# Kernel tuning notes

Measured on AMD Instinct MI355X. Metric: run time of the kernel, lower is better.

Reference implementation:

```python
import jax, jax.numpy as jnp
import numpy as np

B, S, M, D, DI, H, DH, DFF = 2, 1024, 1024, 1024, 1024, 16, 64, 4096
NEG = -1e30


def _ln(x, g, b, eps=1e-5):
    mu = jnp.mean(x, -1, keepdims=True)
    var = jnp.mean((x - mu) ** 2, -1, keepdims=True)
    return (x - mu) / jnp.sqrt(var + eps) * g + b


def _rel_shift(x):
    # x: (b, i, j, h) -- Transformer-XL shift via pad + reshape (exact torch trick)
    b, i, j, h = x.shape
    zp = jnp.zeros((b, 1, j, h), x.dtype)
    xp = jnp.concatenate([zp, x], axis=1).reshape(i + 1, b, j, h)
    return xp[1:].reshape(b, i, j, h)


def setup_inputs() -> dict:
    key = jax.random.key(0)
    ks = jax.random.split(key, 24)
    rn = lambda k, sh, s=1.0: jax.random.normal(k, sh, jnp.float32) * s
    St = S + M
    causal = jnp.arange(St)[None, :] > (jnp.arange(S)[:, None] + M)  # (S, St)
    tgt_mask = jnp.broadcast_to(causal[None, :, :, None], (B, S, St, 1))
    return {
        "x": rn(ks[0], (B, S, D)),
        "enc_output": rn(ks[1], (B, S, D)),
        "pos_emb": rn(ks[2], (St, DI)),
        "u": rn(ks[3], (H, DH), 0.02),
        "v": rn(ks[4], (H, DH), 0.02),
        "mem": rn(ks[5], (B, M, D)),
        "tgt_mask": tgt_mask,
        "Wq_m": rn(ks[6], (D, DI), 0.02),
        "Wkv_m": rn(ks[7], (D, 2 * DI), 0.02),
        "fcw_m": rn(ks[8], (DI, D), 0.02),
        "fcb_m": jnp.zeros((D,), jnp.float32),
        "lnm_g": jnp.ones((D,), jnp.float32),
        "lnm_b": jnp.zeros((D,), jnp.float32),
        "Wq_c": rn(ks[9], (D, DI), 0.02),
        "Wkv_c": rn(ks[10], (D, 2 * DI), 0.02),
        "fcw_c": rn(ks[11], (DI, D), 0.02),
        "fcb_c": jnp.zeros((D,), jnp.float32),
        "lnc_g": jnp.ones((D,), jnp.float32),
        "lnc_b": jnp.zeros((D,), jnp.float32),
        "W1": rn(ks[12], (D, DFF), 0.02),
        "b1": jnp.zeros((DFF,), jnp.float32),
        "W2": rn(ks[13], (DFF, D), 0.02),
        "b2": jnp.zeros((D,), jnp.float32),
        "ln1_g": jnp.ones((D,), jnp.float32),
        "ln1_b": jnp.zeros((D,), jnp.float32),
        "ln2_g": jnp.ones((D,), jnp.float32),
        "ln2_b": jnp.zeros((D,), jnp.float32),
        "ln3_g": jnp.ones((D,), jnp.float32),
        "ln3_b": jnp.zeros((D,), jnp.float32),
    }


def reference(x, enc_output, pos_emb, u, v, mem, tgt_mask,
              Wq_m, Wkv_m, fcw_m, fcb_m, lnm_g, lnm_b,
              Wq_c, Wkv_c, fcw_c, fcb_c, lnc_g, lnc_b,
              W1, b1, W2, b2,
              ln1_g, ln1_b, ln2_g, ln2_b, ln3_g, ln3_b):
    scale = 1.0 / (DH ** 0.5)

    def mha(xn):  # RecurrenceAttention (internal post-norm, pre_norm=False)
        h = jnp.concatenate([mem, xn], axis=1)                       # (B, M+S, D)
        q = (xn @ Wq_m).reshape(B, S, H, DH)
        k, vv = jnp.split(h @ Wkv_m, 2, axis=-1)
        k = k.reshape(B, S + M, H, DH)
        vv = vv.reshape(B, S + M, H, DH)
        content = jnp.einsum('bihd,bjhd->bijh', q + u, k)
        pe = pos_emb.reshape(S + M, H, DH)
        pos = jnp.einsum('bihd,jhd->bijh', q + v, pe)
        attn = content + _rel_shift(pos)
        attn = jnp.where(tgt_mask, NEG, attn)
        attn = attn * scale
        attn = jax.nn.softmax(attn, axis=1)                          # NOTE: query axis (faithful)
        o = jnp.einsum('bijh,bjhd->bihd', attn, vv).reshape(B, S, DI)
        return _ln(xn + o @ fcw_m + fcb_m, lnm_g, lnm_b)

    def cross(dec):  # CrossAttention (internal post-norm)
        q = (dec @ Wq_c).reshape(B, S, H, DH)
        k, vv = jnp.split(enc_output @ Wkv_c, 2, axis=-1)
        k = k.reshape(B, S, H, DH)
        vv = vv.reshape(B, S, H, DH)
        attn = jnp.einsum('bihd,bjhd->bijh', q, k) * scale
        attn = jax.nn.softmax(attn, axis=1)                          # query axis (faithful)
        o = jnp.einsum('bijh,bjhd->bihd', attn, vv).reshape(B, S, DI)
        return _ln(dec + o @ fcw_c + fcb_c, lnc_g, lnc_b)

    # decoder layer, pre_norm=True path
    out = x + mha(_ln(x, ln1_g, ln1_b))
    out2 = out + cross(_ln(out, ln2_g, ln2_b))
    h = jax.nn.gelu(_ln(out2, ln3_g, ln3_b) @ W1 + b1, approximate=False)
    out3 = out2 + (h @ W2 + b2)
    return out3
```

## Files before the change

### kernel.cpp

```cpp
#include <hip/hip_runtime.h>

typedef unsigned short u16;
typedef __attribute__((ext_vector_type(4))) unsigned short u16x4;
typedef __attribute__((ext_vector_type(8))) unsigned short u16x8;
typedef __attribute__((ext_vector_type(8))) __bf16 bf16x8;
typedef __attribute__((ext_vector_type(4))) float f32x4;

#define DEV __device__ __forceinline__

DEV float b2f(u16 u){ union{ unsigned int i; float f; } x; x.i = ((unsigned int)u) << 16; return x.f; }
DEV u16 f2b(float f){ unsigned int x = __float_as_uint(f); return (u16)((x + 0x7fffu + ((x >> 16) & 1u)) >> 16); }

DEV void block_red2(float& s, float& q){
#pragma unroll
  for (int off = 32; off; off >>= 1){ s += __shfl_down(s, off); q += __shfl_down(q, off); }
  __shared__ float sh1[4], sh2[4];
  int lane = threadIdx.x & 63, w = threadIdx.x >> 6;
  if (lane == 0){ sh1[w] = s; sh2[w] = q; }
  __syncthreads();
  s = sh1[0] + sh1[1] + sh1[2] + sh1[3];
  q = sh2[0] + sh2[1] + sh2[2] + sh2[3];
}

template<int WM, int WN, bool OUTB>
__global__ __launch_bounds__(WM*WN*64) void gemm_bt(
    const u16* __restrict__ A, const u16* __restrict__ Bm, void* __restrict__ Cp,
    int K, int lda, int ldb, int ldc, int Hh,
    long aob, long aoh, long bob, long boh, long cob, long coh)
{
  constexpr int BM = WM*64, BN = WN*64, BK = 64, NW = WM*WN;
  __shared__ u16 At[BM*64];
  __shared__ u16 Bt[BN*64];
  int z = blockIdx.z, b_ = z / Hh, h_ = z % Hh;
  const u16* Ab = A + (long)b_*aob + (long)h_*aoh;
  const u16* Bb = Bm + (long)b_*bob + (long)h_*boh;
  long cbase = (long)b_*cob + (long)h_*coh;
  int m0 = blockIdx.y * BM, n0 = blockIdx.x * BN;
  int tid = threadIdx.x, lane = tid & 63, wv = tid >> 6;
  int wm = wv / WN, wn = wv % WN;
  f32x4 acc[4][4];
  f32x4 z4 = {0.f, 0.f, 0.f, 0.f};
#pragma unroll
  for (int a = 0; a < 4; a++)
#pragma unroll
    for (int b = 0; b < 4; b++) acc[a][b] = z4;
  int lr = lane & 15, lk8 = (lane >> 4) * 8;
  int rq = lane >> 3, cq = (lane & 7) << 3;
  for (int k0 = 0; k0 < K; k0 += BK){
    __syncthreads();
#pragma unroll
    for (int q = wv; q < BM/8; q += NW){
      const u16* g = &Ab[(long)(m0 + q*8 + rq)*lda + k0 + cq];
      __builtin_amdgcn_global_load_lds((const __attribute__((address_space(1))) void*)g,
          (__attribute__((address_space(3))) void*)&At[q*512], 16, 0, 0);
    }
#pragma unroll
    for (int q = wv; q < BN/8; q += NW){
      const u16* g = &Bb[(long)(n0 + q*8 + rq)*ldb + k0 + cq];
      __builtin_amdgcn_global_load_lds((const __attribute__((address_space(1))) void*)g,
          (__attribute__((address_space(3))) void*)&Bt[q*512], 16, 0, 0);
    }
    __syncthreads();
#pragma unroll
    for (int kk = 0; kk < BK; kk += 32){
      bf16x8 af[4], bfr[4];
#pragma unroll
      for (int mi = 0; mi < 4; mi++) af[mi]  = *(bf16x8*)&At[(wm*64 + mi*16 + lr)*64 + kk + lk8];
#pragma unroll
      for (int ni = 0; ni < 4; ni++) bfr[ni] = *(bf16x8*)&Bt[(wn*64 + ni*16 + lr)*64 + kk + lk8];
#pragma unroll
      for (int mi = 0; mi < 4; mi++)
#pragma unroll
        for (int ni = 0; ni < 4; ni++)
          acc[mi][ni] = __builtin_amdgcn_mfma_f32_16x16x32_bf16(af[mi], bfr[ni], acc[mi][ni], 0, 0, 0);
    }
  }
  int orow = (lane >> 4) * 4, ocol = lane & 15;
#pragma unroll
  for (int mi = 0; mi < 4; mi++)
#pragma unroll
    for (int ni = 0; ni < 4; ni++){
      int row = m0 + wm*64 + mi*16 + orow;
      int col = n0 + wn*64 + ni*16 + ocol;
      long cidx = cbase + (long)row*ldc + col;
#pragma unroll
      for (int r = 0; r < 4; r++){
        float vv = acc[mi][ni][r];
        if (OUTB) ((u16*)Cp)[cidx + (long)r*ldc] = f2b(vv);
        else      ((float*)Cp)[cidx + (long)r*ldc] = vv;
      }
    }
}

template<int KD, bool MASK>
__global__ __launch_bounds__(256) void attn_passA(
    const u16* __restrict__ Kp, const u16* __restrict__ Qp, float* __restrict__ mz,
    int J, int kld, int qld,
    long kob, long koh, long qob, long qoh, int H, float scale, int mztot)
{
  constexpr int KP = KD + 8;
  constexpr int RCH = KD / 8;
  constexpr int QREG = KD / 16;
  __shared__ u16 Qt[128*KP];
  int bh = blockIdx.y, b = bh / H, h = bh % H;
  const u16* Kb = Kp + (long)b*kob + (long)h*koh;
  const u16* Qb = Qp + (long)b*qob + (long)h*qoh;
  int j0 = blockIdx.x * 64;
  int tid = threadIdx.x, lane = tid & 63, w = tid >> 6;
  int lr = lane & 15, lk8 = (lane >> 4) * 8;
  bf16x8 ak[KD/32];
  {
    const u16* kr = &Kb[(long)(j0 + w*16 + lr)*kld];
#pragma unroll
    for (int kk = 0; kk < KD/32; kk++) ak[kk] = *(const bf16x8*)&kr[kk*32 + lk8];
  }
  float m_run[4], z_run[4];
#pragma unroll
  for (int r = 0; r < 4; r++){ m_run[r] = -3.0e38f; z_run[r] = 0.f; }
  f32x4 zz = {0.f,0.f,0.f,0.f};
  int itLo = 0;
  if (MASK){ int tt = j0 - 1151; itLo = tt > 0 ? (tt + 127)/128 : 0; }
  u16x8 qreg[QREG];
#pragma unroll
  for (int qq = 0; qq < QREG; qq++){
    int idx = tid + qq*256; int r = idx / RCH, c = (idx % RCH) * 8;
    qreg[qq] = *(const u16x8*)&Qb[(long)(itLo*128 + r)*qld + c];
  }
  for (int it = itLo; it < 8; it++){
    __syncthreads();
#pragma unroll
    for (int qq = 0; qq < QREG; qq++){
      int idx = tid + qq*256; int r = idx / RCH, c = (idx % RCH) * 8;
      *(u16x8*)&Qt[r*KP + c] = qreg[qq];
    }
    if (it + 1 < 8){
#pragma unroll
      for (int qq = 0; qq < QREG; qq++){
        int idx = tid + qq*256; int r = idx / RCH, c = (idx % RCH) * 8;
        qreg[qq] = *(const u16x8*)&Qb[(long)((it+1)*128 + r)*qld + c];
      }
    }
    __syncthreads();
    f32x4 acc[8];
#pragma unroll
    for (int ni = 0; ni < 8; ni++) acc[ni] = zz;
#pragma unroll
    for (int kk = 0; kk < KD; kk += 32){
      bf16x8 bq[8];
#pragma unroll
      for (int ni = 0; ni < 8; ni++) bq[ni] = *(bf16x8*)&Qt[(ni*16 + lr)*KP + kk + lk8];
#pragma unroll
      for (int ni = 0; ni < 8; ni++)
        acc[ni] = __builtin_amdgcn_mfma_f32_16x16x32_bf16(ak[kk/32], bq[ni], acc[ni], 0, 0, 0);
    }
#pragma unroll
    for (int r = 0; r < 4; r++){
      int jg = j0 + w*16 + ((lane >> 4) << 2) + r;
      float sv[8]; float tm = -3.0e38f;
#pragma unroll
      for (int ni = 0; ni < 8; ni++){
        int ig = it*128 + ni*16 + (lane & 15);
        float s = acc[ni][r] * scale;
        bool val = (!MASK) || (ig >= jg - 1024);
        sv[ni] = val ? s : -3.0e38f;
        tm = fmaxf(tm, sv[ni]);
      }
#pragma unroll
      for (int off = 1; off < 16; off <<= 1) tm = fmaxf(tm, __shfl_xor(tm, off));
      float mn = fmaxf(m_run[r], tm);
      float zt = 0.f;
#pragma unroll
      for (int ni = 0; ni < 8; ni++)
        zt += (sv[ni] > -1.0e37f) ? __expf(sv[ni] - mn) : 0.f;
#pragma unroll
      for (int off = 1; off < 16; off <<= 1) zt += __shfl_xor(zt, off);
      z_run[r] = z_run[r] * __expf(m_run[r] - mn) + zt;
      m_run[r] = mn;
    }
  }
  if ((lane & 15) == 0){
#pragma unroll
    for (int r = 0; r < 4; r++){
      int jg = j0 + w*16 + ((lane >> 4) << 2) + r;
      mz[(long)bh*J + jg] = m_run[r];
      mz[(long)mztot + (long)bh*J + jg] = 1.f / z_run[r];
    }
  }
}

template<int KD, bool MASK>
__global__ __launch_bounds__(256) void attn_passB(
    const u16* __restrict__ Kp, const u16* __restrict__ Qp, const u16* __restrict__ Vtp,
    const float* __restrict__ mz, float* __restrict__ Op,
    int J, int kld, int qld, int vld, int oldd,
    long kob, long koh, long qob, long qoh, long vob, long voh, long oob, long ooh,
    int H, float scale, int mztot, int jtHalf, long opstride)
{
  constexpr int KP = KD + 8, PSTR = 140, VSTR = 136;
  constexpr int RCH = KD / 8;
  constexpr int KREG = KD / 16;
  __shared__ u16 PK[128*KP];
  __shared__ u16 Vtt[64*VSTR];
  u16* Kt = PK;
  u16* Pt = PK;
  int bh = blockIdx.y, b = bh / H, h = bh % H;
  int jh = blockIdx.z;
  const u16* Kb = Kp + (long)b*kob + (long)h*koh;
  const u16* Qb = Qp + (long)b*qob + (long)h*qoh;
  const u16* Vb = Vtp + (long)b*vob + (long)h*voh;
  float* Ob = Op + (long)jh*opstride + (long)b*oob + (long)h*ooh;
  const float* mzm = mz + (long)bh*J;
  const float* mzz = mz + (long)mztot + (long)bh*J;
  int i0 = blockIdx.x * 64;
  int tid = threadIdx.x, lane = tid & 63, w = tid >> 6;
  int lr = lane & 15, lk8 = (lane >> 4) * 8;
  bf16x8 aq[KD/32];
  {
    const u16* qr = &Qb[(long)(i0 + w*16 + lr)*qld];
#pragma unroll
    for (int kk = 0; kk < KD/32; kk++) aq[kk] = *(const bf16x8*)&qr[kk*32 + lk8];
  }
  f32x4 acc_o[4];
  f32x4 zz = {0.f,0.f,0.f,0.f};
#pragma unroll
  for (int nd = 0; nd < 4; nd++) acc_o[nd] = zz;
  int lo = jh * jtHalf, hi = lo + jtHalf;
  if (MASK){ int lim = (i0 + 1087)/128 + 1; hi = hi < lim ? hi : lim; }
  if (lo < hi){
    u16x8 kreg[KREG];
    u16x8 vreg[4];
#pragma unroll
    for (int qq = 0; qq < KREG; qq++){
      int idx = tid + qq*256; int r = idx / RCH, c = (idx % RCH) * 8;
      kreg[qq] = *(const u16x8*)&Kb[(long)(lo*128 + r)*kld + c];
    }
#pragma unroll
    for (int qq = 0; qq < 4; qq++){
      int idx = tid + qq*256; int r = idx >> 4, c = (idx & 15) << 3;
      vreg[qq] = *(const u16x8*)&Vb[(long)r*vld + lo*128 + c];
    }
    for (int jt = lo; jt < hi; jt++){
      __syncthreads();
#pragma unroll
      for (int qq = 0; qq < KREG; qq++){
        int idx = tid + qq*256; int r = idx / RCH, c = (idx % RCH) * 8;
        *(u16x8*)&Kt[r*KP + c] = kreg[qq];
      }
#pragma unroll
      for (int qq = 0; qq < 4; qq++){
        int idx = tid + qq*256; int r = idx >> 4, c = (idx & 15) << 3;
        *(u16x8*)&Vtt[r*VSTR + c] = vreg[qq];
      }
      if (jt + 1 < hi){
#pragma unroll
        for (int qq = 0; qq < KREG; qq++){
          int idx = tid + qq*256; int r = idx / RCH, c = (idx % RCH) * 8;
          kreg[qq] = *(const u16x8*)&Kb[(long)((jt+1)*128 + r)*kld + c];
        }
#pragma unroll
        for (int qq = 0; qq < 4; qq++){
          int idx = tid + qq*256; int r = idx >> 4, c = (idx & 15) << 3;
          vreg[qq] = *(const u16x8*)&Vb[(long)r*vld + (jt+1)*128 + c];
        }
      }
      __syncthreads();
      float mjv[8], zjv[8];
#pragma unroll
      for (int ni = 0; ni < 8; ni++){
        int jg = jt*128 + ni*16 + (lane & 15);
        mjv[ni] = mzm[jg]; zjv[ni] = mzz[jg];
      }
      f32x4 acc[8];
#pragma unroll
      for (int ni = 0; ni < 8; ni++) acc[ni] = zz;
#pragma unroll
      for (int kk = 0; kk < KD; kk += 32){
        bf16x8 bk[8];
#pragma unroll
        for (int ni = 0; ni < 8; ni++) bk[ni] = *(bf16x8*)&Kt[(ni*16 + lr)*KP + kk + lk8];
#pragma unroll
        for (int ni = 0; ni < 8; ni++)
          acc[ni] = __builtin_amdgcn_mfma_f32_16x16x32_bf16(aq[kk/32], bk[ni], acc[ni], 0, 0, 0);
      }
      __syncthreads();
#pragma unroll
      for (int ni = 0; ni < 8; ni++){
        int jg = jt*128 + ni*16 + (lane & 15);
#pragma unroll
        for (int r = 0; r < 4; r++){
          int ig = i0 + w*16 + ((lane >> 4) << 2) + r;
          bool val = (!MASK) || (ig >= jg - 1024);
          float p = val ? __expf(acc[ni][r] * scale - mjv[ni]) * zjv[ni] : 0.f;
          Pt[(w*16 + ((lane >> 4) << 2) + r)*PSTR + ni*16 + (lane & 15)] = f2b(p);
        }
      }
#pragma unroll
      for (int kk = 0; kk < 128; kk += 32){
        bf16x8 pa, vb[4];
        pa = *(bf16x8*)&Pt[(w*16 + lr)*PSTR + kk + lk8];
#pragma unroll
        for (int nd = 0; nd < 4; nd++) vb[nd] = *(bf16x8*)&Vtt[(nd*16 + lr)*VSTR + kk + lk8];
#pragma unroll
        for (int nd = 0; nd < 4; nd++)
          acc_o[nd] = __builtin_amdgcn_mfma_f32_16x16x32_bf16(pa, vb[nd], acc_o[nd], 0, 0, 0);
      }
    }
  }
#pragma unroll
  for (int nd = 0; nd < 4; nd++)
#pragma unroll
    for (int r = 0; r < 4; r++){
      int ig = i0 + w*16 + ((lane >> 4) << 2) + r;
      int d = nd*16 + (lane & 15);
      Ob[(long)ig*oldd + d] = acc_o[nd][r];
    }
}

__global__ __launch_bounds__(256) void combine_o(const float* __restrict__ p, u16* __restrict__ o)
{
  const long PS = 2097152;
  long i = ((long)blockIdx.x*256 + threadIdx.x) * 4;
  const float* a = &p[i];
  const float* b = &p[i + PS];
  u16x4 r;
#pragma unroll
  for (int e = 0; e < 4; e++) r[e] = f2b(a[e] + b[e]);
  *(u16x4*)&o[i] = r;
}

__global__ __launch_bounds__(256) void transpose_k(
    const u16* __restrict__ src, u16* __restrict__ dst,
    int lds_, int ldd, int Hh, long sob, long soh, long dob, long doh)
{
  __shared__ u16 tile[64*72];
  int z = blockIdx.z, b_ = z / Hh, h_ = z % Hh;
  const u16* S_ = src + (long)b_*sob + (long)h_*soh;
  u16* D_ = dst + (long)b_*dob + (long)h_*doh;
  int r0 = blockIdx.y * 64, c0 = blockIdx.x * 64;
  int tid = threadIdx.x;
  for (int idx = tid; idx < 512; idx += 256){
    int r = idx >> 3, c = (idx & 7) << 3;
    *(u16x8*)&tile[r*72 + c] = *(const u16x8*)&S_[(long)(r0 + r)*lds_ + c0 + c];
  }
  __syncthreads();
  for (int idx = tid; idx < 512; idx += 256){
    int c = idx >> 3, r = (idx & 7) << 3;
    u16x8 v;
#pragma unroll
    for (int e = 0; e < 8; e++) v[e] = tile[(r + e)*72 + c];
    *(u16x8*)&D_[(long)(c0 + c)*ldd + r0 + r] = v;
  }
}

__global__ __launch_bounds__(256) void transpose_cvt_k(
    const float* __restrict__ src, u16* __restrict__ dst, int lds_, int ldd)
{
  __shared__ u16 tile[64*72];
  int r0 = blockIdx.y * 64, c0 = blockIdx.x * 64;
  int tid = threadIdx.x;
  for (int idx = tid; idx < 512; idx += 256){
    int r = idx >> 3, c = (idx & 7) << 3;
    const float* s = &src[(long)(r0 + r)*lds_ + c0 + c];
#pragma unroll
    for (int e = 0; e < 8; e++) tile[r*72 + c + e] = f2b(s[e]);
  }
  __syncthreads();
  for (int idx = tid; idx < 512; idx += 256){
    int c = idx >> 3, r = (idx & 7) << 3;
    u16x8 v;
#pragma unroll
    for (int e = 0; e < 8; e++) v[e] = tile[(r + e)*72 + c];
    *(u16x8*)&dst[(long)(c0 + c)*ldd + r0 + r] = v;
  }
}

__global__ __launch_bounds__(256) void cvt_k(const float* __restrict__ src, u16* __restrict__ dst)
{
  long i = ((long)blockIdx.x*256 + threadIdx.x) * 4;
  float4 v = *(const float4*)&src[i];
  u16x4 o; o[0] = f2b(v.x); o[1] = f2b(v.y); o[2] = f2b(v.z); o[3] = f2b(v.w);
  *(u16x4*)&dst[i] = o;
}

__global__ __launch_bounds__(256) void ln_k(const float* __restrict__ src, const float* __restrict__ g,
                                            const float* __restrict__ be, u16* __restrict__ out)
{
  long base = (long)blockIdx.x * 1024;
  int tid = threadIdx.x;
  const float* s = src + base + tid*4;
  float v[4] = {s[0], s[1], s[2], s[3]};
  float s1 = v[0]+v[1]+v[2]+v[3];
  float s2 = v[0]*v[0]+v[1]*v[1]+v[2]*v[2]+v[3]*v[3];
  block_red2(s1, s2);
  float mu = s1 * (1.f/1024.f);
  float var = s2 * (1.f/1024.f) - mu*mu;
  float rs = rsqrtf(var + 1e-5f);
#pragma unroll
  for (int e = 0; e < 4; e++){
    int col = tid*4 + e;
    out[base + col] = f2b((v[e]-mu)*rs*g[col] + be[col]);
  }
}

__global__ __launch_bounds__(256) void add_ln_k(const float* __restrict__ go,
    const u16* __restrict__ xn, const float* __restrict__ bias,
    const float* __restrict__ g, const float* __restrict__ be,
    const float* __restrict__ resid, float* __restrict__ outp)
{
  const long PS = 2097152;
// ... 46 lines not shown
  int bj = blockIdx.x;
  int j = bj & 2047;
  long kvrow = (long)bj * 2048;
  long obase = (long)bj * 2048;
  for (int t = threadIdx.x; t < 2048; t += 256){
    int h = t >> 7, e = t & 127;
    u16 val = (e < 64) ? kv[kvrow + h*64 + e] : f2b(pe[(long)j*1024 + h*64 + (e - 64)]);
    BB[obase + t] = val;
  }
}

__global__ __launch_bounds__(256) void gelu_k(const float* __restrict__ f1, const float* __restrict__ b1,
                                              u16* __restrict__ h1)
{
  long i = (long)blockIdx.x*256 + threadIdx.x;
  float x = f1[i] + b1[i & 4095];
  h1[i] = f2b(0.5f * x * (1.f + erff(x * 0.70710678118654752f)));
}

__global__ __launch_bounds__(256) void final_k(const float* __restrict__ out2, const float* __restrict__ f2,
                                               const float* __restrict__ b2v, float* __restrict__ outp)
{
  const long PS = 2097152;
  long i = (long)blockIdx.x*256 + threadIdx.x;
  outp[i] = out2[i] + f2[i] + f2[i + PS] + f2[i + 2*PS] + f2[i + 3*PS] + b2v[i & 1023];
}

extern "C" void kernel_launch(void* const* d_in, const int* in_sizes, int n_in,
                              void* d_out, int out_size, void* d_ws, size_t ws_size,
                              hipStream_t stream)
{
  (void)in_sizes; (void)n_in; (void)out_size; (void)ws_size;
  const float* X    = (const float*)d_in[0];
  const float* ENC  = (const float*)d_in[1];
  const float* PE   = (const float*)d_in[2];
  const float* Uu   = (const float*)d_in[3];
  const float* Vv   = (const float*)d_in[4];
  const float* MEM  = (const float*)d_in[5];
  const float* WQM  = (const float*)d_in[7];
  const float* WKVM = (const float*)d_in[8];
  const float* FCWM = (const float*)d_in[9];
  const float* FCBM = (const float*)d_in[10];
  const float* LNMG = (const float*)d_in[11];
  const float* LNMB = (const float*)d_in[12];
  const float* WQC  = (const float*)d_in[13];
  const float* WKVC = (const float*)d_in[14];
  const float* FCWC = (const float*)d_in[15];
  const float* FCBC = (const float*)d_in[16];
  const float* LNCG = (const float*)d_in[17];
  const float* LNCB = (const float*)d_in[18];
  const float* W1   = (const float*)d_in[19];
  const float* B1   = (const float*)d_in[20];
  const float* W2   = (const float*)d_in[21];
  const float* B2   = (const float*)d_in[22];
  const float* LN1G = (const float*)d_in[23];
  const float* LN1B = (const float*)d_in[24];
  const float* LN2G = (const float*)d_in[25];
  const float* LN2B = (const float*)d_in[26];
  const float* LN3G = (const float*)d_in[27];
  const float* LN3B = (const float*)d_in[28];
  float* OUT = (float*)d_out;
  char* W = (char*)d_ws;
  const size_t MB = 1ull << 20;

  u16*   wT_a  = (u16*)(W + 0*MB);
  u16*   wT_b  = (u16*)(W + 2*MB);
  u16*   wT_c  = (u16*)(W + 6*MB);
  u16*   w1T   = (u16*)(W + 0*MB);
  u16*   xn1   = (u16*)(W + 8*MB);
  u16*   q     = (u16*)(W + 12*MB);
  u16*   o_b   = (u16*)(W + 12*MB);
  u16*   kv    = (u16*)(W + 16*MB);
  float* outb  = (float*)(W + 24*MB);
  u16*   QQ    = (u16*)(W + 32*MB);
  u16*   xn2   = (u16*)(W + 32*MB);
  u16*   qc    = (u16*)(W + 36*MB);
  u16*   BB    = (u16*)(W + 40*MB);
  u16*   kvc   = (u16*)(W + 40*MB);
  u16*   Vtc   = (u16*)(W + 48*MB);
  u16*   oc    = (u16*)(W + 52*MB);
  u16*   Vt    = (u16*)(W + 56*MB);
  u16*   w2T   = (u16*)(W + 56*MB);
  float* mzb   = (float*)(W + 64*MB);
  u16*   memb  = (u16*)(W + 68*MB);
  u16*   encb  = (u16*)(W + 68*MB);
  float* opart = (float*)(W + 66*MB);
  float* ofc   = (float*)(W + 66*MB);
  float* f1    = (float*)(W + 66*MB);
  float* f2    = (float*)(W + 66*MB);
  u16*   h1    = (u16*)(W + 98*MB);
  float* out2b = (float*)(W + 114*MB);

  transpose_cvt_k<<<dim3(16,16),256,0,stream>>>(WQM,  wT_a, 1024,1024);
  transpose_cvt_k<<<dim3(32,16),256,0,stream>>>(WKVM, wT_b, 2048,1024);
  transpose_cvt_k<<<dim3(16,16),256,0,stream>>>(FCWM, wT_c, 1024,1024);
  cvt_k<<<2048,256,0,stream>>>(MEM, memb);
  ln_k<<<2048,256,0,stream>>>(X, LN1G, LN1B, xn1);
  gemm_bt<2,2,true><<<dim3(8,16,1),256,0,stream>>>(xn1, wT_a, q, 1024, 1024,1024,1024, 1, 0,0,0,0,0,0);
  gemm_bt<2,2,true><<<dim3(16,8,2),256,0,stream>>>(memb, wT_b, kv, 1024, 1024,1024,2048, 1,
      1048576,0, 0,0, 4194304,0);
  gemm_bt<2,2,true><<<dim3(16,8,2),256,0,stream>>>(xn1, wT_b, kv + (size_t)1024*2048, 1024, 1024,1024,2048, 1,
      1048576,0, 0,0, 4194304,0);
  build_qq<<<2048,256,0,stream>>>(q, Uu, Vv, QQ);
  build_bb<<<4096,256,0,stream>>>(kv, PE, BB);
  transpose_k<<<dim3(1,32,32),256,0,stream>>>(kv + 1024, Vt, 2048, 2048, 16,
      4194304,64, 2097152,131072);
  attn_passA<128,true><<<dim3(32,32),256,0,stream>>>(BB, QQ, mzb, 2048, 2048, 2048,
      4194304,128, 2097152,128, 16, 0.125f, 65536);
  attn_passB<128,true><<<dim3(16,32,2),256,0,stream>>>(BB, QQ, Vt, mzb, opart, 2048,
      2048,2048,2048,1024, 4194304,128, 2097152,128, 2097152,131072, 1048576,64, 16, 0.125f, 65536,
      8, 2097152);
  combine_o<<<2048,256,0,stream>>>(opart, o_b);
  gemm_bt<2,2,false><<<dim3(8,16,4),256,0,stream>>>(o_b, wT_c, ofc, 256, 1024,1024,1024, 4,
      0,256, 0,256, 0,2097152);
  add_ln_k<<<2048,256,0,stream>>>(ofc, xn1, FCBM, LNMG, LNMB, X, outb);

  transpose_cvt_k<<<dim3(16,16),256,0,stream>>>(WQC,  wT_a, 1024,1024);
  transpose_cvt_k<<<dim3(32,16),256,0,stream>>>(WKVC, wT_b, 2048,1024);
  transpose_cvt_k<<<dim3(16,16),256,0,stream>>>(FCWC, wT_c, 1024,1024);
  cvt_k<<<2048,256,0,stream>>>(ENC, encb);
  ln_k<<<2048,256,0,stream>>>(outb, LN2G, LN2B, xn2);
  gemm_bt<2,2,true><<<dim3(8,16,1),256,0,stream>>>(xn2, wT_a, qc, 1024, 1024,1024,1024, 1, 0,0,0,0,0,0);
  gemm_bt<2,2,true><<<dim3(16,16,1),256,0,stream>>>(encb, wT_b, kvc, 1024, 1024,1024,2048, 1, 0,0,0,0,0,0);
  transpose_k<<<dim3(1,16,32),256,0,stream>>>(kvc + 1024, Vtc, 2048, 1024, 16,
      2097152,64, 1048576,65536);
  attn_passA<64,false><<<dim3(16,32),256,0,stream>>>(kvc, qc, mzb, 1024, 2048, 1024,
      2097152,64, 1048576,64, 16, 0.125f, 32768);
  attn_passB<64,false><<<dim3(16,32,2),256,0,stream>>>(kvc, qc, Vtc, mzb, opart, 1024,
      2048,1024,1024,1024, 2097152,64, 1048576,64, 1048576,65536, 1048576,64, 16, 0.125f, 32768,
      4, 2097152);
  combine_o<<<2048,256,0,stream>>>(opart, oc);
  gemm_bt<2,2,false><<<dim3(8,16,4),256,0,stream>>>(oc, wT_c, ofc, 256, 1024,1024,1024, 4,
      0,256, 0,256, 0,2097152);
  add_ln_k<<<2048,256,0,stream>>>(ofc, xn2, FCBC, LNCG, LNCB, outb, out2b);

  transpose_cvt_k<<<dim3(64,16),256,0,stream>>>(W1, w1T, 4096,1024);
  transpose_cvt_k<<<dim3(16,64),256,0,stream>>>(W2, w2T, 1024,4096);
  ln_k<<<2048,256,0,stream>>>(out2b, LN3G, LN3B, xn2);
  gemm_bt<2,2,false><<<dim3(32,16,1),256,0,stream>>>(xn2, w1T, f1, 1024, 1024,1024,4096, 1, 0,0,0,0,0,0);
  gelu_k<<<32768,256,0,stream>>>(f1, B1, h1);
  gemm_bt<2,2,false><<<dim3(8,16,4),256,0,stream>>>(h1, w2T, f2, 1024, 4096,4096,1024, 4,
      0,1024, 0,1024, 0,2097152);
  final_k<<<8192,256,0,stream>>>(out2b, f2, B2, OUT);
}
```

Before: 676.3 us.

## Double per-wave row tile in attention passes to reuse shared-memory K/Q tiles

Both attention passes now have each wave own 32 rows (two 16-row MFMA subtiles) instead of 16, so each block covers 128 rows and the grids are halved. Every B-operand fragment loaded from LDS (Q, K, V tiles) feeds twice as many MFMAs, cutting LDS and global reloads per unit of work. In exchange, register pressure roughly doubles for accumulators and A fragments, and fewer blocks are launched, which can reduce occupancy and load balance, especially for the causal-masked pass. The P buffer stride was also changed from 140 to 136 so that 128 P rows fit in the shared buffer.

```diff
diff --git a/kernel.cpp b/kernel.cpp
--- a/kernel.cpp
+++ b/kernel.cpp
@@ -105,18 +105,21 @@
   int bh = blockIdx.y, b = bh / H, h = bh % H;
   const u16* Kb = Kp + (long)b*kob + (long)h*koh;
   const u16* Qb = Qp + (long)b*qob + (long)h*qoh;
-  int j0 = blockIdx.x * 64;
+  int j0 = blockIdx.x * 128;
   int tid = threadIdx.x, lane = tid & 63, w = tid >> 6;
   int lr = lane & 15, lk8 = (lane >> 4) * 8;
-  bf16x8 ak[KD/32];
-  {
-    const u16* kr = &Kb[(long)(j0 + w*16 + lr)*kld];
-#pragma unroll
-    for (int kk = 0; kk < KD/32; kk++) ak[kk] = *(const bf16x8*)&kr[kk*32 + lk8];
-  }
-  float m_run[4], z_run[4];
-#pragma unroll
-  for (int r = 0; r < 4; r++){ m_run[r] = -3.0e38f; z_run[r] = 0.f; }
+  bf16x8 ak[2][KD/32];
+#pragma unroll
+  for (int mj = 0; mj < 2; mj++){
+    const u16* kr = &Kb[(long)(j0 + w*32 + mj*16 + lr)*kld];
+#pragma unroll
+    for (int kk = 0; kk < KD/32; kk++) ak[mj][kk] = *(const bf16x8*)&kr[kk*32 + lk8];
+  }
+  float m_run[2][4], z_run[2][4];
+#pragma unroll
+  for (int mj = 0; mj < 2; mj++)
+#pragma unroll
+    for (int r = 0; r < 4; r++){ m_run[mj][r] = -3.0e38f; z_run[mj][r] = 0.f; }
   f32x4 zz = {0.f,0.f,0.f,0.f};
   int itLo = 0;
   if (MASK){ int tt = j0 - 1151; itLo = tt > 0 ? (tt + 127)/128 : 0; }
@@ -141,49 +144,57 @@
       }
     }
     __syncthreads();
-    f32x4 acc[8];
-#pragma unroll
-    for (int ni = 0; ni < 8; ni++) acc[ni] = zz;
-#pragma unroll
-    for (int kk = 0; kk < KD; kk += 32){
+    f32x4 acc[2][8];
+#pragma unroll
+    for (int mj = 0; mj < 2; mj++)
+#pragma unroll
+      for (int ni = 0; ni < 8; ni++) acc[mj][ni] = zz;
+#pragma unroll
+    for (int kk8 = 0; kk8 < KD/32; kk8++){
       bf16x8 bq[8];
 #pragma unroll
-      for (int ni = 0; ni < 8; ni++) bq[ni] = *(bf16x8*)&Qt[(ni*16 + lr)*KP + kk + lk8];
-#pragma unroll
-      for (int ni = 0; ni < 8; ni++)
-        acc[ni] = __builtin_amdgcn_mfma_f32_16x16x32_bf16(ak[kk/32], bq[ni], acc[ni], 0, 0, 0);
-    }
+      for (int ni = 0; ni < 8; ni++) bq[ni] = *(bf16x8*)&Qt[(ni*16 + lr)*KP + kk8*32 + lk8];
+#pragma unroll
+      for (int mj = 0; mj < 2; mj++)
+#pragma unroll
+        for (int ni = 0; ni < 8; ni++)
+          acc[mj][ni] = __builtin_amdgcn_mfma_f32_16x16x32_bf16(ak[mj][kk8], bq[ni], acc[mj][ni], 0, 0, 0);
+    }
+#pragma unroll
+    for (int mj = 0; mj < 2; mj++)
 #pragma unroll
     for (int r = 0; r < 4; r++){
-      int jg = j0 + w*16 + ((lane >> 4) << 2) + r;
+      int jg = j0 + w*32 + mj*16 + ((lane >> 4) << 2) + r;
       float sv[8]; float tm = -3.0e38f;
 #pragma unroll
       for (int ni = 0; ni < 8; ni++){
         int ig = it*128 + ni*16 + (lane & 15);
-        float s = acc[ni][r] * scale;
+        float s = acc[mj][ni][r] * scale;
         bool val = (!MASK) || (ig >= jg - 1024);
         sv[ni] = val ? s : -3.0e38f;
         tm = fmaxf(tm, sv[ni]);
       }
 #pragma unroll
       for (int off = 1; off < 16; off <<= 1) tm = fmaxf(tm, __shfl_xor(tm, off));
-      float mn = fmaxf(m_run[r], tm);
+      float mn = fmaxf(m_run[mj][r], tm);
       float zt = 0.f;
 #pragma unroll
       for (int ni = 0; ni < 8; ni++)
         zt += (sv[ni] > -1.0e37f) ? __expf(sv[ni] - mn) : 0.f;
 #pragma unroll
       for (int off = 1; off < 16; off <<= 1) zt += __shfl_xor(zt, off);
-      z_run[r] = z_run[r] * __expf(m_run[r] - mn) + zt;
-      m_run[r] = mn;
+      z_run[mj][r] = z_run[mj][r] * __expf(m_run[mj][r] - mn) + zt;
+      m_run[mj][r] = mn;
     }
   }
   if ((lane & 15) == 0){
 #pragma unroll
+    for (int mj = 0; mj < 2; mj++)
+#pragma unroll
     for (int r = 0; r < 4; r++){
-      int jg = j0 + w*16 + ((lane >> 4) << 2) + r;
-      mz[(long)bh*J + jg] = m_run[r];
-      mz[(long)mztot + (long)bh*J + jg] = 1.f / z_run[r];
+      int jg = j0 + w*32 + mj*16 + ((lane >> 4) << 2) + r;
+      mz[(long)bh*J + jg] = m_run[mj][r];
+      mz[(long)mztot + (long)bh*J + jg] = 1.f / z_run[mj][r];
     }
   }
 }
@@ -196,10 +207,10 @@
     long kob, long koh, long qob, long qoh, long vob, long voh, long oob, long ooh,
     int H, float scale, int mztot, int jtHalf, long opstride)
 {
-  constexpr int KP = KD + 8, PSTR = 140, VSTR = 136;
+  constexpr int KP = KD + 8, PSTR = 136, VSTR = 136;
   constexpr int RCH = KD / 8;
   constexpr int KREG = KD / 16;
-  __shared__ u16 PK[128*KP];
+  __shared__ u16 PK[128*136];
   __shared__ u16 Vtt[64*VSTR];
   u16* Kt = PK;
   u16* Pt = PK;
@@ -211,19 +222,22 @@
   float* Ob = Op + (long)jh*opstride + (long)b*oob + (long)h*ooh;
   const float* mzm = mz + (long)bh*J;
   const float* mzz = mz + (long)mztot + (long)bh*J;
-  int i0 = blockIdx.x * 64;
+  int i0 = blockIdx.x * 128;
   int tid = threadIdx.x, lane = tid & 63, w = tid >> 6;
   int lr = lane & 15, lk8 = (lane >> 4) * 8;
-  bf16x8 aq[KD/32];
-  {
-    const u16* qr = &Qb[(long)(i0 + w*16 + lr)*qld];
-#pragma unroll
-    for (int kk = 0; kk < KD/32; kk++) aq[kk] = *(const bf16x8*)&qr[kk*32 + lk8];
-  }
-  f32x4 acc_o[4];
+  bf16x8 aq[2][KD/32];
+#pragma unroll
+  for (int mi = 0; mi < 2; mi++){
+    const u16* qr = &Qb[(long)(i0 + w*32 + mi*16 + lr)*qld];
+#pragma unroll
+    for (int kk = 0; kk < KD/32; kk++) aq[mi][kk] = *(const bf16x8*)&qr[kk*32 + lk8];
+  }
+  f32x4 acc_o[2][4];
   f32x4 zz = {0.f,0.f,0.f,0.f};
 #pragma unroll
-  for (int nd = 0; nd < 4; nd++) acc_o[nd] = zz;
+  for (int mi = 0; mi < 2; mi++)
+#pragma unroll
+    for (int nd = 0; nd < 4; nd++) acc_o[mi][nd] = zz;
   int lo = jh * jtHalf, hi = lo + jtHalf;
   if (MASK){ int lim = (i0 + 1087)/128 + 1; hi = hi < lim ? hi : lim; }
   if (lo < hi){
@@ -270,49 +284,60 @@
         int jg = jt*128 + ni*16 + (lane & 15);
         mjv[ni] = mzm[jg]; zjv[ni] = mzz[jg];
       }
-      f32x4 acc[8];
-#pragma unroll
-      for (int ni = 0; ni < 8; ni++) acc[ni] = zz;
-#pragma unroll
-      for (int kk = 0; kk < KD; kk += 32){
+      f32x4 acc[2][8];
+#pragma unroll
+      for (int mi = 0; mi < 2; mi++)
+#pragma unroll
+        for (int ni = 0; ni < 8; ni++) acc[mi][ni] = zz;
+#pragma unroll
+      for (int kk8 = 0; kk8 < KD/32; kk8++){
         bf16x8 bk[8];
 #pragma unroll
-        for (int ni = 0; ni < 8; ni++) bk[ni] = *(bf16x8*)&Kt[(ni*16 + lr)*KP + kk + lk8];
-#pragma unroll
-        for (int ni = 0; ni < 8; ni++)
-          acc[ni] = __builtin_amdgcn_mfma_f32_16x16x32_bf16(aq[kk/32], bk[ni], acc[ni], 0, 0, 0);
+        for (int ni = 0; ni < 8; ni++) bk[ni] = *(bf16x8*)&Kt[(ni*16 + lr)*KP + kk8*32 + lk8];
+#pragma unroll
+        for (int mi = 0; mi < 2; mi++)
+#pragma unroll
+          for (int ni = 0; ni < 8; ni++)
+            acc[mi][ni] = __builtin_amdgcn_mfma_f32_16x16x32_bf16(aq[mi][kk8], bk[ni], acc[mi][ni], 0, 0, 0);
       }
       __syncthreads();
+#pragma unroll
+      for (int mi = 0; mi < 2; mi++)
 #pragma unroll
       for (int ni = 0; ni < 8; ni++){
         int jg = jt*128 + ni*16 + (lane & 15);
 #pragma unroll
         for (int r = 0; r < 4; r++){
-          int ig = i0 + w*16 + ((lane >> 4) << 2) + r;
+          int ig = i0 + w*32 + mi*16 + ((lane >> 4) << 2) + r;
           bool val = (!MASK) || (ig >= jg - 1024);
-          float p = val ? __expf(acc[ni][r] * scale - mjv[ni]) * zjv[ni] : 0.f;
-          Pt[(w*16 + ((lane >> 4) << 2) + r)*PSTR + ni*16 + (lane & 15)] = f2b(p);
+          float p = val ? __expf(acc[mi][ni][r] * scale - mjv[ni]) * zjv[ni] : 0.f;
+          Pt[(w*32 + mi*16 + ((lane >> 4) << 2) + r)*PSTR + ni*16 + (lane & 15)] = f2b(p);
         }
       }
 #pragma unroll
       for (int kk = 0; kk < 128; kk += 32){
-        bf16x8 pa, vb[4];
-        pa = *(bf16x8*)&Pt[(w*16 + lr)*PSTR + kk + lk8];
+        bf16x8 pa[2], vb[4];
 #pragma unroll
         for (int nd = 0; nd < 4; nd++) vb[nd] = *(bf16x8*)&Vtt[(nd*16 + lr)*VSTR + kk + lk8];
 #pragma unroll
-        for (int nd = 0; nd < 4; nd++)
-          acc_o[nd] = __builtin_amdgcn_mfma_f32_16x16x32_bf16(pa, vb[nd], acc_o[nd], 0, 0, 0);
-      }
-    }
-  }
+        for (int mi = 0; mi < 2; mi++) pa[mi] = *(bf16x8*)&Pt[(w*32 + mi*16 + lr)*PSTR + kk + lk8];
+#pragma unroll
+        for (int mi = 0; mi < 2; mi++)
+#pragma unroll
+          for (int nd = 0; nd < 4; nd++)
+            acc_o[mi][nd] = __builtin_amdgcn_mfma_f32_16x16x32_bf16(pa[mi], vb[nd], acc_o[mi][nd], 0, 0, 0);
+      }
+    }
+  }
+#pragma unroll
+  for (int mi = 0; mi < 2; mi++)
 #pragma unroll
   for (int nd = 0; nd < 4; nd++)
 #pragma unroll
     for (int r = 0; r < 4; r++){
-      int ig = i0 + w*16 + ((lane >> 4) << 2) + r;
+      int ig = i0 + w*32 + mi*16 + ((lane >> 4) << 2) + r;
       int d = nd*16 + (lane & 15);
-      Ob[(long)ig*oldd + d] = acc_o[nd][r];
+      Ob[(long)ig*oldd + d] = acc_o[mi][nd][r];
     }
 }
 
@@ -560,9 +585,9 @@
   build_bb<<<4096,256,0,stream>>>(kv, PE, BB);
   transpose_k<<<dim3(1,32,32),256,0,stream>>>(kv + 1024, Vt, 2048, 2048, 16,
       4194304,64, 2097152,131072);
-  attn_passA<128,true><<<dim3(32,32),256,0,stream>>>(BB, QQ, mzb, 2048, 2048, 2048,
+  attn_passA<128,true><<<dim3(16,32),256,0,stream>>>(BB, QQ, mzb, 2048, 2048, 2048,
       4194304,128, 2097152,128, 16, 0.125f, 65536);
-  attn_passB<128,true><<<dim3(16,32,2),256,0,stream>>>(BB, QQ, Vt, mzb, opart, 2048,
+  attn_passB<128,true><<<dim3(8,32,2),256,0,stream>>>(BB, QQ, Vt, mzb, opart, 2048,
       2048,2048,2048,1024, 4194304,128, 2097152,128, 2097152,131072, 1048576,64, 16, 0.125f, 65536,
       8, 2097152);
   combine_o<<<2048,256,0,stream>>>(opart, o_b);
@@ -579,9 +604,9 @@
   gemm_bt<2,2,true><<<dim3(16,16,1),256,0,stream>>>(encb, wT_b, kvc, 1024, 1024,1024,2048, 1, 0,0,0,0,0,0);
   transpose_k<<<dim3(1,16,32),256,0,stream>>>(kvc + 1024, Vtc, 2048, 1024, 16,
       2097152,64, 1048576,65536);
-  attn_passA<64,false><<<dim3(16,32),256,0,stream>>>(kvc, qc, mzb, 1024, 2048, 1024,
+  attn_passA<64,false><<<dim3(8,32),256,0,stream>>>(kvc, qc, mzb, 1024, 2048, 1024,
       2097152,64, 1048576,64, 16, 0.125f, 32768);
-  attn_passB<64,false><<<dim3(16,32,2),256,0,stream>>>(kvc, qc, Vtc, mzb, opart, 1024,
+  attn_passB<64,false><<<dim3(8,32,2),256,0,stream>>>(kvc, qc, Vtc, mzb, opart, 1024,
       2048,1024,1024,1024, 2097152,64, 1048576,64, 1048576,65536, 1048576,64, 16, 0.125f, 32768,
       4, 2097152);
   combine_o<<<2048,256,0,stream>>>(opart, oc);
```

Result: no change. 683.8 us (+1.1%).

## Double-buffer attention pass B with 64-key tiles and four-way key split

Applied to the files above, without the earlier changes.

Rewrites the attention pass-B kernel to use 64-key tiles with double-buffered K/V shared-memory stages. This cuts per-iteration barriers from three to one, so the next tile's stores overlap the current tile's compute. The self-attention launch now splits the key range four ways instead of two, and combine_o is templated on the number of partials. The goal is more blocks in flight and less synchronisation stall. The cost is more partial-output traffic to write and re-read in the combine step.

```diff
diff --git a/kernel.cpp b/kernel.cpp
--- a/kernel.cpp
+++ b/kernel.cpp
@@ -194,15 +194,14 @@
     const float* __restrict__ mz, float* __restrict__ Op,
     int J, int kld, int qld, int vld, int oldd,
     long kob, long koh, long qob, long qoh, long vob, long voh, long oob, long ooh,
-    int H, float scale, int mztot, int jtHalf, long opstride)
-{
-  constexpr int KP = KD + 8, PSTR = 140, VSTR = 136;
+    int H, float scale, int mztot, int jtCnt, long opstride)
+{
+  constexpr int KP = KD + 8, VSTR = 72, PSTR = 72;
   constexpr int RCH = KD / 8;
-  constexpr int KREG = KD / 16;
-  __shared__ u16 PK[128*KP];
-  __shared__ u16 Vtt[64*VSTR];
-  u16* Kt = PK;
-  u16* Pt = PK;
+  constexpr int KREG = RCH / 4;
+  __shared__ u16 Kt[2][64*KP];
+  __shared__ u16 Vtt[2][64*VSTR];
+  __shared__ u16 Pt[64*PSTR];
   int bh = blockIdx.y, b = bh / H, h = bh % H;
   int jh = blockIdx.z;
   const u16* Kb = Kp + (long)b*kob + (long)h*koh;
@@ -224,86 +223,99 @@
   f32x4 zz = {0.f,0.f,0.f,0.f};
 #pragma unroll
   for (int nd = 0; nd < 4; nd++) acc_o[nd] = zz;
-  int lo = jh * jtHalf, hi = lo + jtHalf;
-  if (MASK){ int lim = (i0 + 1087)/128 + 1; hi = hi < lim ? hi : lim; }
+  int lo = jh * jtCnt, hi = lo + jtCnt;
+  if (MASK){ int lim = (i0 + 1087)/64 + 1; hi = hi < lim ? hi : lim; }
   if (lo < hi){
-    u16x8 kreg[KREG];
-    u16x8 vreg[4];
+    u16x8 kreg[KREG], vreg[2];
 #pragma unroll
     for (int qq = 0; qq < KREG; qq++){
       int idx = tid + qq*256; int r = idx / RCH, c = (idx % RCH) * 8;
-      kreg[qq] = *(const u16x8*)&Kb[(long)(lo*128 + r)*kld + c];
-    }
-#pragma unroll
-    for (int qq = 0; qq < 4; qq++){
-      int idx = tid + qq*256; int r = idx >> 4, c = (idx & 15) << 3;
-      vreg[qq] = *(const u16x8*)&Vb[(long)r*vld + lo*128 + c];
-    }
+      kreg[qq] = *(const u16x8*)&Kb[(long)(lo*64 + r)*kld + c];
+    }
+#pragma unroll
+    for (int qq = 0; qq < 2; qq++){
+      int idx = tid + qq*256; int r = idx >> 3, c = (idx & 7) << 3;
+      vreg[qq] = *(const u16x8*)&Vb[(long)r*vld + lo*64 + c];
+    }
+#pragma unroll
+    for (int qq = 0; qq < KREG; qq++){
+      int idx = tid + qq*256; int r = idx / RCH, c = (idx % RCH) * 8;
+      *(u16x8*)&Kt[0][r*KP + c] = kreg[qq];
+    }
+#pragma unroll
+    for (int qq = 0; qq < 2; qq++){
+      int idx = tid + qq*256; int r = idx >> 3, c = (idx & 7) << 3;
+      *(u16x8*)&Vtt[0][r*VSTR + c] = vreg[qq];
+    }
+    __syncthreads();
+    int cur = 0;
     for (int jt = lo; jt < hi; jt++){
-      __syncthreads();
-#pragma unroll
-      for (int qq = 0; qq < KREG; qq++){
-        int idx = tid + qq*256; int r = idx / RCH, c = (idx % RCH) * 8;
-        *(u16x8*)&Kt[r*KP + c] = kreg[qq];
-      }
-#pragma unroll
-      for (int qq = 0; qq < 4; qq++){
-        int idx = tid + qq*256; int r = idx >> 4, c = (idx & 15) << 3;
-        *(u16x8*)&Vtt[r*VSTR + c] = vreg[qq];
-      }
-      if (jt + 1 < hi){
+      bool pf = (jt + 1 < hi);
+      if (pf){
 #pragma unroll
         for (int qq = 0; qq < KREG; qq++){
           int idx = tid + qq*256; int r = idx / RCH, c = (idx % RCH) * 8;
-          kreg[qq] = *(const u16x8*)&Kb[(long)((jt+1)*128 + r)*kld + c];
+          kreg[qq] = *(const u16x8*)&Kb[(long)((jt+1)*64 + r)*kld + c];
         }
 #pragma unroll
-        for (int qq = 0; qq < 4; qq++){
-          int idx = tid + qq*256; int r = idx >> 4, c = (idx & 15) << 3;
-          vreg[qq] = *(const u16x8*)&Vb[(long)r*vld + (jt+1)*128 + c];
+        for (int qq = 0; qq < 2; qq++){
+          int idx = tid + qq*256; int r = idx >> 3, c = (idx & 7) << 3;
+          vreg[qq] = *(const u16x8*)&Vb[(long)r*vld + (jt+1)*64 + c];
         }
       }
-      __syncthreads();
-      float mjv[8], zjv[8];
-#pragma unroll
-      for (int ni = 0; ni < 8; ni++){
-        int jg = jt*128 + ni*16 + (lane & 15);
+      float mjv[4], zjv[4];
+#pragma unroll
+      for (int ni = 0; ni < 4; ni++){
+        int jg = jt*64 + ni*16 + lr;
         mjv[ni] = mzm[jg]; zjv[ni] = mzz[jg];
       }
-      f32x4 acc[8];
-#pragma unroll
-      for (int ni = 0; ni < 8; ni++) acc[ni] = zz;
-#pragma unroll
-      for (int kk = 0; kk < KD; kk += 32){
-        bf16x8 bk[8];
-#pragma unroll
-        for (int ni = 0; ni < 8; ni++) bk[ni] = *(bf16x8*)&Kt[(ni*16 + lr)*KP + kk + lk8];
-#pragma unroll
-        for (int ni = 0; ni < 8; ni++)
-          acc[ni] = __builtin_amdgcn_mfma_f32_16x16x32_bf16(aq[kk/32], bk[ni], acc[ni], 0, 0, 0);
-      }
-      __syncthreads();
-#pragma unroll
-      for (int ni = 0; ni < 8; ni++){
-        int jg = jt*128 + ni*16 + (lane & 15);
+      f32x4 acc[4];
+#pragma unroll
+      for (int ni = 0; ni < 4; ni++) acc[ni] = zz;
+#pragma unroll
+      for (int kk8 = 0; kk8 < KD/32; kk8++){
+        bf16x8 bk[4];
+#pragma unroll
+        for (int ni = 0; ni < 4; ni++) bk[ni] = *(bf16x8*)&Kt[cur][(ni*16 + lr)*KP + kk8*32 + lk8];
+#pragma unroll
+        for (int ni = 0; ni < 4; ni++)
+          acc[ni] = __builtin_amdgcn_mfma_f32_16x16x32_bf16(aq[kk8], bk[ni], acc[ni], 0, 0, 0);
+      }
+#pragma unroll
+      for (int ni = 0; ni < 4; ni++){
+        int jg = jt*64 + ni*16 + lr;
 #pragma unroll
         for (int r = 0; r < 4; r++){
           int ig = i0 + w*16 + ((lane >> 4) << 2) + r;
           bool val = (!MASK) || (ig >= jg - 1024);
           float p = val ? __expf(acc[ni][r] * scale - mjv[ni]) * zjv[ni] : 0.f;
-          Pt[(w*16 + ((lane >> 4) << 2) + r)*PSTR + ni*16 + (lane & 15)] = f2b(p);
+          Pt[(w*16 + ((lane >> 4) << 2) + r)*PSTR + ni*16 + lr] = f2b(p);
         }
       }
-#pragma unroll
-      for (int kk = 0; kk < 128; kk += 32){
+      if (pf){
+#pragma unroll
+        for (int qq = 0; qq < KREG; qq++){
+          int idx = tid + qq*256; int r = idx / RCH, c = (idx % RCH) * 8;
+          *(u16x8*)&Kt[cur^1][r*KP + c] = kreg[qq];
+        }
+#pragma unroll
+        for (int qq = 0; qq < 2; qq++){
+          int idx = tid + qq*256; int r = idx >> 3, c = (idx & 7) << 3;
+          *(u16x8*)&Vtt[cur^1][r*VSTR + c] = vreg[qq];
+        }
+      }
+#pragma unroll
+      for (int kk = 0; kk < 64; kk += 32){
         bf16x8 pa, vb[4];
+#pragma unroll
+        for (int nd = 0; nd < 4; nd++) vb[nd] = *(bf16x8*)&Vtt[cur][(nd*16 + lr)*VSTR + kk + lk8];
         pa = *(bf16x8*)&Pt[(w*16 + lr)*PSTR + kk + lk8];
-#pragma unroll
-        for (int nd = 0; nd < 4; nd++) vb[nd] = *(bf16x8*)&Vtt[(nd*16 + lr)*VSTR + kk + lk8];
 #pragma unroll
         for (int nd = 0; nd < 4; nd++)
           acc_o[nd] = __builtin_amdgcn_mfma_f32_16x16x32_bf16(pa, vb[nd], acc_o[nd], 0, 0, 0);
       }
+      __syncthreads();
+      cur ^= 1;
     }
   }
 #pragma unroll
@@ -316,15 +328,19 @@
     }
 }
 
+template<int NP>
 __global__ __launch_bounds__(256) void combine_o(const float* __restrict__ p, u16* __restrict__ o)
 {
   const long PS = 2097152;
   long i = ((long)blockIdx.x*256 + threadIdx.x) * 4;
-  const float* a = &p[i];
-  const float* b = &p[i + PS];
   u16x4 r;
 #pragma unroll
-  for (int e = 0; e < 4; e++) r[e] = f2b(a[e] + b[e]);
+  for (int e = 0; e < 4; e++){
+    float a = p[i + e];
+#pragma unroll
+    for (int q = 1; q < NP; q++) a += p[i + e + (long)q*PS];
+    r[e] = f2b(a);
+  }
   *(u16x4*)&o[i] = r;
 }
 
@@ -562,10 +578,10 @@
       4194304,64, 2097152,131072);
   attn_passA<128,true><<<dim3(32,32),256,0,stream>>>(BB, QQ, mzb, 2048, 2048, 2048,
       4194304,128, 2097152,128, 16, 0.125f, 65536);
-  attn_passB<128,true><<<dim3(16,32,2),256,0,stream>>>(BB, QQ, Vt, mzb, opart, 2048,
+  attn_passB<128,true><<<dim3(16,32,4),256,0,stream>>>(BB, QQ, Vt, mzb, opart, 2048,
       2048,2048,2048,1024, 4194304,128, 2097152,128, 2097152,131072, 1048576,64, 16, 0.125f, 65536,
       8, 2097152);
-  combine_o<<<2048,256,0,stream>>>(opart, o_b);
+  combine_o<4><<<2048,256,0,stream>>>(opart, o_b);
   gemm_bt<2,2,false><<<dim3(8,16,4),256,0,stream>>>(o_b, wT_c, ofc, 256, 1024,1024,1024, 4,
       0,256, 0,256, 0,2097152);
   add_ln_k<<<2048,256,0,stream>>>(ofc, xn1, FCBM, LNMG, LNMB, X, outb);
@@ -583,8 +599,8 @@
       2097152,64, 1048576,64, 16, 0.125f, 32768);
   attn_passB<64,false><<<dim3(16,32,2),256,0,stream>>>(kvc, qc, Vtc, mzb, opart, 1024,
       2048,1024,1024,1024, 2097152,64, 1048576,64, 1048576,65536, 1048576,64, 16, 0.125f, 32768,
-      4, 2097152);
-  combine_o<<<2048,256,0,stream>>>(opart, oc);
+      8, 2097152);
+  combine_o<2><<<2048,256,0,stream>>>(opart, oc);
   gemm_bt<2,2,false><<<dim3(8,16,4),256,0,stream>>>(oc, wT_c, ofc, 256, 1024,1024,1024, 4,
       0,256, 0,256, 0,2097152);
   add_ln_k<<<2048,256,0,stream>>>(ofc, xn2, FCBC, LNCG, LNCB, outb, out2b);
```

Measured after the change: 678.0 us. No clear change (+0.2%).

## Split attention pass A over two query-tile halves and interleave pass B tiles

Applied to the files above, without the earlier changes.

Pass A (the per-key softmax max/sum over the query axis) now runs with a second grid dimension. Each block takes every other 128-row query tile and writes partial max and sum values, which a new combine_mz kernel merges. This doubles the number of blocks for a grid that was previously small, and balances the causal mask work. Pass B now gives its two split blocks interleaved key tiles instead of contiguous halves, so masked work is shared evenly between them. The cost is an extra small kernel launch and extra partial-buffer traffic.

```diff
diff --git a/kernel.cpp b/kernel.cpp
--- a/kernel.cpp
+++ b/kernel.cpp
@@ -96,13 +96,14 @@
 __global__ __launch_bounds__(256) void attn_passA(
     const u16* __restrict__ Kp, const u16* __restrict__ Qp, float* __restrict__ mz,
     int J, int kld, int qld,
-    long kob, long koh, long qob, long qoh, int H, float scale, int mztot)
+    long kob, long koh, long qob, long qoh, int H, float scale, int mztot, long pstr)
 {
   constexpr int KP = KD + 8;
   constexpr int RCH = KD / 8;
   constexpr int QREG = KD / 16;
   __shared__ u16 Qt[128*KP];
   int bh = blockIdx.y, b = bh / H, h = bh % H;
+  int iz = blockIdx.z;
   const u16* Kb = Kp + (long)b*kob + (long)h*koh;
   const u16* Qb = Qp + (long)b*qob + (long)h*qoh;
   int j0 = blockIdx.x * 64;
@@ -120,24 +121,27 @@
   f32x4 zz = {0.f,0.f,0.f,0.f};
   int itLo = 0;
   if (MASK){ int tt = j0 - 1151; itLo = tt > 0 ? (tt + 127)/128 : 0; }
+  int itStart = (itLo <= iz) ? iz : itLo + ((iz + itLo) & 1);
   u16x8 qreg[QREG];
-#pragma unroll
-  for (int qq = 0; qq < QREG; qq++){
-    int idx = tid + qq*256; int r = idx / RCH, c = (idx % RCH) * 8;
-    qreg[qq] = *(const u16x8*)&Qb[(long)(itLo*128 + r)*qld + c];
-  }
-  for (int it = itLo; it < 8; it++){
+  if (itStart < 8){
+#pragma unroll
+    for (int qq = 0; qq < QREG; qq++){
+      int idx = tid + qq*256; int r = idx / RCH, c = (idx % RCH) * 8;
+      qreg[qq] = *(const u16x8*)&Qb[(long)(itStart*128 + r)*qld + c];
+    }
+  }
+  for (int it = itStart; it < 8; it += 2){
     __syncthreads();
 #pragma unroll
     for (int qq = 0; qq < QREG; qq++){
       int idx = tid + qq*256; int r = idx / RCH, c = (idx % RCH) * 8;
       *(u16x8*)&Qt[r*KP + c] = qreg[qq];
     }
-    if (it + 1 < 8){
+    if (it + 2 < 8){
 #pragma unroll
       for (int qq = 0; qq < QREG; qq++){
         int idx = tid + qq*256; int r = idx / RCH, c = (idx % RCH) * 8;
-        qreg[qq] = *(const u16x8*)&Qb[(long)((it+1)*128 + r)*qld + c];
+        qreg[qq] = *(const u16x8*)&Qb[(long)((it+2)*128 + r)*qld + c];
       }
     }
     __syncthreads();
@@ -178,13 +182,30 @@
       m_run[r] = mn;
     }
   }
+  float* mzp = mz + (long)iz * pstr;
   if ((lane & 15) == 0){
 #pragma unroll
     for (int r = 0; r < 4; r++){
       int jg = j0 + w*16 + ((lane >> 4) << 2) + r;
-      mz[(long)bh*J + jg] = m_run[r];
-      mz[(long)mztot + (long)bh*J + jg] = 1.f / z_run[r];
-    }
+      mzp[(long)bh*J + jg] = m_run[r];
+      mzp[(long)mztot + (long)bh*J + jg] = z_run[r];
+    }
+  }
+}
+
+__global__ __launch_bounds__(256) void combine_mz(const float* __restrict__ p, float* __restrict__ o,
+                                                  int tot, long pstr)
+{
+  int i = blockIdx.x*1024 + threadIdx.x*4;
+#pragma unroll
+  for (int e = 0; e < 4; e++){
+    int idx = i + e;
+    float m0 = p[idx], z0 = p[tot + idx];
+    float m1 = p[pstr + idx], z1 = p[pstr + tot + idx];
+    float m = fmaxf(m0, m1);
+    float z = z0*__expf(m0 - m) + z1*__expf(m1 - m);
+    o[idx] = m;
+    o[tot + idx] = 1.f / z;
   }
 }
 
@@ -194,7 +215,7 @@
     const float* __restrict__ mz, float* __restrict__ Op,
     int J, int kld, int qld, int vld, int oldd,
     long kob, long koh, long qob, long qoh, long vob, long voh, long oob, long ooh,
-    int H, float scale, int mztot, int jtHalf, long opstride)
+    int H, float scale, int mztot, int jtNS, int jtTot, long opstride)
 {
   constexpr int KP = KD + 8, PSTR = 140, VSTR = 136;
   constexpr int RCH = KD / 8;
@@ -224,22 +245,22 @@
   f32x4 zz = {0.f,0.f,0.f,0.f};
 #pragma unroll
   for (int nd = 0; nd < 4; nd++) acc_o[nd] = zz;
-  int lo = jh * jtHalf, hi = lo + jtHalf;
+  int hi = jtTot;
   if (MASK){ int lim = (i0 + 1087)/128 + 1; hi = hi < lim ? hi : lim; }
-  if (lo < hi){
+  if (jh < hi){
     u16x8 kreg[KREG];
     u16x8 vreg[4];
 #pragma unroll
     for (int qq = 0; qq < KREG; qq++){
       int idx = tid + qq*256; int r = idx / RCH, c = (idx % RCH) * 8;
-      kreg[qq] = *(const u16x8*)&Kb[(long)(lo*128 + r)*kld + c];
+      kreg[qq] = *(const u16x8*)&Kb[(long)(jh*128 + r)*kld + c];
     }
 #pragma unroll
     for (int qq = 0; qq < 4; qq++){
       int idx = tid + qq*256; int r = idx >> 4, c = (idx & 15) << 3;
-      vreg[qq] = *(const u16x8*)&Vb[(long)r*vld + lo*128 + c];
-    }
-    for (int jt = lo; jt < hi; jt++){
+      vreg[qq] = *(const u16x8*)&Vb[(long)r*vld + jh*128 + c];
+    }
+    for (int jt = jh; jt < hi; jt += jtNS){
       __syncthreads();
 #pragma unroll
       for (int qq = 0; qq < KREG; qq++){
@@ -251,16 +272,16 @@
         int idx = tid + qq*256; int r = idx >> 4, c = (idx & 15) << 3;
         *(u16x8*)&Vtt[r*VSTR + c] = vreg[qq];
       }
-      if (jt + 1 < hi){
+      if (jt + jtNS < hi){
 #pragma unroll
         for (int qq = 0; qq < KREG; qq++){
           int idx = tid + qq*256; int r = idx / RCH, c = (idx % RCH) * 8;
-          kreg[qq] = *(const u16x8*)&Kb[(long)((jt+1)*128 + r)*kld + c];
+          kreg[qq] = *(const u16x8*)&Kb[(long)((jt+jtNS)*128 + r)*kld + c];
         }
 #pragma unroll
         for (int qq = 0; qq < 4; qq++){
           int idx = tid + qq*256; int r = idx >> 4, c = (idx & 15) << 3;
-          vreg[qq] = *(const u16x8*)&Vb[(long)r*vld + (jt+1)*128 + c];
+          vreg[qq] = *(const u16x8*)&Vb[(long)r*vld + (jt+jtNS)*128 + c];
         }
       }
       __syncthreads();
@@ -316,15 +337,19 @@
     }
 }
 
+template<int NP>
 __global__ __launch_bounds__(256) void combine_o(const float* __restrict__ p, u16* __restrict__ o)
 {
   const long PS = 2097152;
   long i = ((long)blockIdx.x*256 + threadIdx.x) * 4;
-  const float* a = &p[i];
-  const float* b = &p[i + PS];
   u16x4 r;
 #pragma unroll
-  for (int e = 0; e < 4; e++) r[e] = f2b(a[e] + b[e]);
+  for (int e = 0; e < 4; e++){
+    float a = p[i + e];
+#pragma unroll
+    for (int q = 1; q < NP; q++) a += p[i + e + (long)q*PS];
+    r[e] = f2b(a);
+  }
   *(u16x4*)&o[i] = r;
 }
 
@@ -537,6 +562,7 @@
   u16*   Vt    = (u16*)(W + 56*MB);
   u16*   w2T   = (u16*)(W + 56*MB);
   float* mzb   = (float*)(W + 64*MB);
+  float* mzp   = (float*)(W + 65*MB);
   u16*   memb  = (u16*)(W + 68*MB);
   u16*   encb  = (u16*)(W + 68*MB);
   float* opart = (float*)(W + 66*MB);
@@ -560,12 +586,13 @@
   build_bb<<<4096,256,0,stream>>>(kv, PE, BB);
   transpose_k<<<dim3(1,32,32),256,0,stream>>>(kv + 1024, Vt, 2048, 2048, 16,
       4194304,64, 2097152,131072);
-  attn_passA<128,true><<<dim3(32,32),256,0,stream>>>(BB, QQ, mzb, 2048, 2048, 2048,
-      4194304,128, 2097152,128, 16, 0.125f, 65536);
+  attn_passA<128,true><<<dim3(32,32,2),256,0,stream>>>(BB, QQ, mzp, 2048, 2048, 2048,
+      4194304,128, 2097152,128, 16, 0.125f, 65536, 131072);
+  combine_mz<<<64,256,0,stream>>>(mzp, mzb, 65536, 131072);
   attn_passB<128,true><<<dim3(16,32,2),256,0,stream>>>(BB, QQ, Vt, mzb, opart, 2048,
       2048,2048,2048,1024, 4194304,128, 2097152,128, 2097152,131072, 1048576,64, 16, 0.125f, 65536,
-      8, 2097152);
-  combine_o<<<2048,256,0,stream>>>(opart, o_b);
+      2, 16, 2097152);
+  combine_o<2><<<2048,256,0,stream>>>(opart, o_b);
   gemm_bt<2,2,false><<<dim3(8,16,4),256,0,stream>>>(o_b, wT_c, ofc, 256, 1024,1024,1024, 4,
       0,256, 0,256, 0,2097152);
   add_ln_k<<<2048,256,0,stream>>>(ofc, xn1, FCBM, LNMG, LNMB, X, outb);
@@ -579,12 +606,13 @@
   gemm_bt<2,2,true><<<dim3(16,16,1),256,0,stream>>>(encb, wT_b, kvc, 1024, 1024,1024,2048, 1, 0,0,0,0,0,0);
   transpose_k<<<dim3(1,16,32),256,0,stream>>>(kvc + 1024, Vtc, 2048, 1024, 16,
       2097152,64, 1048576,65536);
-  attn_passA<64,false><<<dim3(16,32),256,0,stream>>>(kvc, qc, mzb, 1024, 2048, 1024,
-      2097152,64, 1048576,64, 16, 0.125f, 32768);
+  attn_passA<64,false><<<dim3(16,32,2),256,0,stream>>>(kvc, qc, mzp, 1024, 2048, 1024,
+      2097152,64, 1048576,64, 16, 0.125f, 32768, 65536);
+  combine_mz<<<32,256,0,stream>>>(mzp, mzb, 32768, 65536);
   attn_passB<64,false><<<dim3(16,32,2),256,0,stream>>>(kvc, qc, Vtc, mzb, opart, 1024,
       2048,1024,1024,1024, 2097152,64, 1048576,64, 1048576,65536, 1048576,64, 16, 0.125f, 32768,
-      4, 2097152);
-  combine_o<<<2048,256,0,stream>>>(opart, oc);
+      2, 8, 2097152);
+  combine_o<2><<<2048,256,0,stream>>>(opart, oc);
   gemm_bt<2,2,false><<<dim3(8,16,4),256,0,stream>>>(oc, wT_c, ofc, 256, 1024,1024,1024, 4,
       0,256, 0,256, 0,2097152);
   add_ln_k<<<2048,256,0,stream>>>(ofc, xn2, FCBC, LNCG, LNCB, outb, out2b);
```

Result: no change. 678.6 us (+0.3%).
